# Kernel tuning notes

Hardware: AMD Instinct MI355X
Metric: run time of the kernel (lower is better)

Reference implementation:

```python
import jax, jax.numpy as jnp
import numpy as np

H = 20          # hidden_size
IN = 2          # GRU input / l1 output dim


def setup_inputs() -> dict:
    key = jax.random.key(0)
    ks = jax.random.split(key, 7)
    B = 32768
    s = 1.0 / np.sqrt(H)  # torch default init scale
    hidden = jax.random.normal(ks[0], (1, B, H), dtype=jnp.float32)
    w_ih = jax.random.uniform(ks[1], (3 * H, IN), jnp.float32, -s, s)
    w_hh = jax.random.uniform(ks[2], (3 * H, H), jnp.float32, -s, s)
    b_ih = jax.random.uniform(ks[3], (3 * H,), jnp.float32, -s, s)
    b_hh = jax.random.uniform(ks[4], (3 * H,), jnp.float32, -s, s)
    w_l = jax.random.uniform(ks[5], (IN, H), jnp.float32, -s, s)
    b_l = jax.random.uniform(ks[6], (IN,), jnp.float32, -s, s)
    return {"hidden": hidden, "w_ih": w_ih, "w_hh": w_hh,
            "b_ih": b_ih, "b_hh": b_hh, "w_l": w_l, "b_l": b_l,
            "step": 200}


def reference(hidden, w_ih, w_hh, b_ih, b_hh, w_l, b_l, step):
    reverse = True
    B = hidden.shape[1]
    h0 = hidden[0]                      # [B, H]
    x0 = jnp.zeros((B, IN), hidden.dtype)  # first GRU input is zeros

    def gru_step(carry, _):
        h, x = carry
        gi = x @ w_ih.T + b_ih          # [B, 3H]
        gh = h @ w_hh.T + b_hh          # [B, 3H]
        ir, iz, inn = jnp.split(gi, 3, axis=-1)
        hr, hz, hn = jnp.split(gh, 3, axis=-1)
        r = jax.nn.sigmoid(ir + hr)
        z = jax.nn.sigmoid(iz + hz)
        n = jnp.tanh(inn + r * hn)
        h_new = (1.0 - z) * n + z * h   # [B, H]
        y = h_new @ w_l.T + b_l         # [B, 2] -> next input
        return (h_new, y), y

    (_, _), ys = jax.lax.scan(gru_step, (h0, x0), None, length=step)
    # ys: [step, B, 2]; original appends per-step then reverses the list
    if reverse:
        ys = ys[::-1]
    return jnp.transpose(ys, (1, 0, 2))  # [B, step, 2]
```

## Files before the change

### kernel.cpp

```cpp
#include <hip/hip_runtime.h>

#define HDIM 20
#define BLOCK 256

typedef __fp16 half8 __attribute__((ext_vector_type(8)));
typedef __fp16 half2v __attribute__((ext_vector_type(2)));
typedef float  float4v __attribute__((ext_vector_type(4)));
typedef int    int4v  __attribute__((ext_vector_type(4)));

static __device__ __forceinline__ float4v mfma16(half8 a, half8 b, float4v c) {
    return __builtin_amdgcn_mfma_f32_16x16x32_f16(a, b, c, 0, 0, 0);
}


__global__ __launch_bounds__(BLOCK, 2) void gru_decoder_kernel(
    const float* __restrict__ hidden,
    const float* __restrict__ w_ih,
    const float* __restrict__ w_hh,
    const float* __restrict__ b_ih,
    const float* __restrict__ b_hh,
    const float* __restrict__ w_l,
    const float* __restrict__ b_l,
    const int*  __restrict__ step_ptr,
    float* __restrict__ out,
    int B)
{
    const int tid = threadIdx.x;
    const int l   = tid & 63;
    const int wv  = tid >> 6;
    const int el  = l & 15;
    const int q   = l >> 4;
    const int e   = (blockIdx.x * 4 + wv) * 16 + el;
    const int step = *step_ptr;

    const float NL2E  = -1.4426950408889634f;
    const float T2L2E =  2.8853900817779268f;

    const int u_dst = el >> 2;
    const int g     = el & 3;

    half8 Afold[5], Azero[5], Ay;
    #pragma unroll
    for (int T = 0; T < 5; ++T) {
        const int u  = 4 * T + u_dst;
        const int rr = (g == 0) ? u : (g == 1) ? 20 + u : 40 + u;
        const float sc = (g <= 1) ? NL2E : T2L2E;
        half8 hf, h0;
        #pragma unroll
        for (int j = 0; j < 8; ++j) {
            float af = 0.f, a0 = 0.f;
            if (j < 5) {
                const int uk = 4 * j + q;
                float wx = w_ih[rr * 2 + 0] * w_l[uk] + w_ih[rr * 2 + 1] * w_l[HDIM + uk];
                float wh = w_hh[rr * HDIM + uk];
                if (g <= 1)      { af = wh + wx; a0 = wh; }
                else if (g == 2) { af = wx;      a0 = 0.f; }
                else             { af = wh;      a0 = wh; }
            } else if (j == 7 && q == 0) {
                float bx = w_ih[rr * 2 + 0] * b_l[0] + w_ih[rr * 2 + 1] * b_l[1];
                if (g <= 1)      { af = b_ih[rr] + b_hh[rr] + bx; a0 = b_ih[rr] + b_hh[rr]; }
                else if (g == 2) { af = b_ih[rr] + bx;            a0 = b_ih[rr]; }
                else             { af = b_hh[rr];                 a0 = b_hh[rr]; }
            }
            hf[j] = (__fp16)(af * sc);
            h0[j] = (__fp16)(a0 * sc);
        }
        Afold[T] = hf;
        Azero[T] = h0;
    }
    {
        half8 hy;
        #pragma unroll
        for (int j = 0; j < 8; ++j) {
            float v = 0.f;
            if (el < 2) {
                if (j < 5)                 v = w_l[el * HDIM + 4 * j + q];
                else if (j == 7 && q == 0) v = b_l[el];
            }
            hy[j] = (__fp16)v;
        }
        Ay = hy;
    }

    int w3const;
    {
        half2v c67; c67[0] = (__fp16)0.f; c67[1] = (__fp16)((q == 0) ? 1.f : 0.f);
        w3const = __builtin_bit_cast(int, c67);
    }

    float hprev[5];
    half8 Bf;
    {
        const float* hb = hidden + (size_t)e * HDIM;
        #pragma unroll
        for (int T = 0; T < 5; ++T) hprev[T] = hb[4 * T + q];
        int4v bi;
        bi[0] = __builtin_bit_cast(int, __builtin_amdgcn_cvt_pkrtz(hprev[0], hprev[1]));
        bi[1] = __builtin_bit_cast(int, __builtin_amdgcn_cvt_pkrtz(hprev[2], hprev[3]));
        bi[2] = __builtin_bit_cast(int, __builtin_amdgcn_cvt_pkrtz(hprev[4], 0.f));
        bi[3] = w3const;
        Bf = __builtin_bit_cast(half8, bi);
    }

    const float4v czero = {0.f, 0.f, 0.f, 0.f};
    float4v C[5];

    auto issue_gates = [&](const half8* A) {
        #pragma unroll
        for (int T = 0; T < 5; ++T) C[T] = mfma16(A[T], Bf, czero);
    };
    auto finish_update = [&]() {
        #pragma unroll
        for (int T = 0; T < 5; ++T) {
            float r = __builtin_amdgcn_rcpf(1.f + __builtin_amdgcn_exp2f(C[T][0]));
            float z = __builtin_amdgcn_rcpf(1.f + __builtin_amdgcn_exp2f(C[T][1]));
            float npre2 = __builtin_fmaf(r, C[T][3], C[T][2]);
            float tn = __builtin_amdgcn_rcpf(1.f + __builtin_amdgcn_exp2f(npre2));
            float n = __builtin_fmaf(-2.f, tn, 1.f);
            hprev[T] = __builtin_fmaf(z, hprev[T] - n, n);
        }
        int4v bi;
        bi[0] = __builtin_bit_cast(int, __builtin_amdgcn_cvt_pkrtz(hprev[0], hprev[1]));
        bi[1] = __builtin_bit_cast(int, __builtin_amdgcn_cvt_pkrtz(hprev[2], hprev[3]));
        bi[2] = __builtin_bit_cast(int, __builtin_amdgcn_cvt_pkrtz(hprev[4], 0.f));
        bi[3] = w3const;
        Bf = __builtin_bit_cast(half8, bi);
    };

    float* outp = out + (size_t)e * 2 * step;

    issue_gates(Azero);
    finish_update();

    if ((step & 1) || step < 4) {
        for (int t = 1; t < step; ++t) {
            issue_gates(Afold);
            float4v cy = mfma16(Ay, Bf, czero);
            if (q == 0) {
                float2 st; st.x = cy[0]; st.y = cy[1];
                *(float2*)(outp + 2 * (step - t)) = st;
            }
            finish_update();
        }
        float4v cy = mfma16(Ay, Bf, czero);
        if (q == 0) {
            float2 st; st.x = cy[0]; st.y = cy[1];
            *(float2*)(outp) = st;
        }
        return;
    }

    float4v pend;
    float*  pendp;

    {
        issue_gates(Afold);
        float4v cyA = mfma16(Ay, Bf, czero);
        finish_update();
        issue_gates(Afold);
        float4v cyB = mfma16(Ay, Bf, czero);
        finish_update();
        pend[0] = cyB[0]; pend[1] = cyB[1]; pend[2] = cyA[0]; pend[3] = cyA[1];
        pendp = outp + 2 * (step - 2);
    }

    for (int k = step - 3; k >= 3; k -= 2) {
        issue_gates(Afold);
        float4v cyA = mfma16(Ay, Bf, czero);
        if (q == 0) *(float4v*)pendp = pend;
        finish_update();
        issue_gates(Afold);
        float4v cyB = mfma16(Ay, Bf, czero);
        finish_update();
        pend[0] = cyB[0]; pend[1] = cyB[1]; pend[2] = cyA[0]; pend[3] = cyA[1];
        pendp = outp + 2 * (k - 1);
    }

    {
        issue_gates(Afold);
        float4v cyA = mfma16(Ay, Bf, czero);
        if (q == 0) *(float4v*)pendp = pend;
        finish_update();
        float4v cyB = mfma16(Ay, Bf, czero);
        if (q == 0) {
            float4v st; st[0] = cyB[0]; st[1] = cyB[1]; st[2] = cyA[0]; st[3] = cyA[1];
            *(float4v*)outp = st;
        }
    }
}

extern "C" void kernel_launch(void* const* d_in, const int* in_sizes, int n_in,
                              void* d_out, int out_size, void* d_ws, size_t ws_size,
                              hipStream_t stream) {
    const float* hidden = (const float*)d_in[0];
    const float* w_ih   = (const float*)d_in[1];
    const float* w_hh   = (const float*)d_in[2];
    const float* b_ih   = (const float*)d_in[3];
    const float* b_hh   = (const float*)d_in[4];
    const float* w_l    = (const float*)d_in[5];
    const float* b_l    = (const float*)d_in[6];
    const int*   step   = (const int*)d_in[7];
    float* out = (float*)d_out;

    int B = in_sizes[0] / HDIM;
    int grid = B / 64;

    gru_decoder_kernel<<<grid, BLOCK, 0, stream>>>(
        hidden, w_ih, w_hh, b_ih, b_hh, w_l, b_l, step, out, B);
}
```

Measured before the change: 167.0 us.

## Batch reciprocals via shared-denominator trick and stagger block start with sleep

Rewrites the gate nonlinearity so that pairs of reciprocals share one rcp of their product, applied to the r/z sigmoids and to pairs of tanh denominators. This cuts transcendental-unit instructions per step in exchange for extra multiplies, and risks overflow when exp2 values are large, since the product of two denominators can reach inf. Odd groups of eight blocks also sleep briefly at start to desynchronise waves, so MFMA and transcendental phases interleave across waves on a CU.

```diff
diff --git a/kernel.cpp b/kernel.cpp
--- a/kernel.cpp
+++ b/kernel.cpp
@@ -110,14 +110,33 @@
         for (int T = 0; T < 5; ++T) C[T] = mfma16(A[T], Bf, czero);
     };
     auto finish_update = [&]() {
+        float zz[5], en[5];
         #pragma unroll
         for (int T = 0; T < 5; ++T) {
-            float r = __builtin_amdgcn_rcpf(1.f + __builtin_amdgcn_exp2f(C[T][0]));
-            float z = __builtin_amdgcn_rcpf(1.f + __builtin_amdgcn_exp2f(C[T][1]));
+            float er = __builtin_amdgcn_exp2f(C[T][0]);
+            float ez = __builtin_amdgcn_exp2f(C[T][1]);
+            float ar = 1.f + er;
+            float az = 1.f + ez;
+            float inv = __builtin_amdgcn_rcpf(ar * az);
+            float r  = az * inv;
+            zz[T]    = ar * inv;
             float npre2 = __builtin_fmaf(r, C[T][3], C[T][2]);
-            float tn = __builtin_amdgcn_rcpf(1.f + __builtin_amdgcn_exp2f(npre2));
-            float n = __builtin_fmaf(-2.f, tn, 1.f);
-            hprev[T] = __builtin_fmaf(z, hprev[T] - n, n);
+            en[T] = 1.f + __builtin_amdgcn_exp2f(npre2);
+        }
+        float tn[5];
+        {
+            float i01 = __builtin_amdgcn_rcpf(en[0] * en[1]);
+            tn[0] = en[1] * i01;
+            tn[1] = en[0] * i01;
+            float i23 = __builtin_amdgcn_rcpf(en[2] * en[3]);
+            tn[2] = en[3] * i23;
+            tn[3] = en[2] * i23;
+            tn[4] = __builtin_amdgcn_rcpf(en[4]);
+        }
+        #pragma unroll
+        for (int T = 0; T < 5; ++T) {
+            float n = __builtin_fmaf(-2.f, tn[T], 1.f);
+            hprev[T] = __builtin_fmaf(zz[T], hprev[T] - n, n);
         }
         int4v bi;
         bi[0] = __builtin_bit_cast(int, __builtin_amdgcn_cvt_pkrtz(hprev[0], hprev[1]));
@@ -128,6 +147,8 @@
     };
 
     float* outp = out + (size_t)e * 2 * step;
+
+    if ((blockIdx.x >> 3) & 1) __builtin_amdgcn_s_sleep(10);
 
     issue_gates(Azero);
     finish_update();
```

Result: no change. 169.0 us (+1.2%).

## Replace z and tanh transcendentals with shared-memory lookup tables

Applied to the files above, without the earlier changes.

Builds 64KB LDS lookup tables for sigmoid and tanh at kernel start. The weights are pre-scaled by 2048 and the MFMA accumulator gets an offset, so the z gate and the n-gate activation become a clamped byte offset plus one LDS load instead of exp2 and rcp. It also raises wave priority around the MFMA issue. The aim is fewer transcendental instructions on the serial recurrence path, at the cost of LDS latency and occupancy (64KB per block), quantization error from the 1/512 step and the fp16 scaled weights, and table-build overhead.

```diff
diff --git a/kernel.cpp b/kernel.cpp
--- a/kernel.cpp
+++ b/kernel.cpp
@@ -25,7 +25,19 @@
     float* __restrict__ out,
     int B)
 {
+    __shared__ float lut[16384];
+
     const int tid = threadIdx.x;
+
+    for (int i = tid; i < 8192; i += BLOCK) {
+        float x = (i - 4096) * (1.0f / 512.0f);
+        float es = __builtin_amdgcn_exp2f(-1.4426950408889634f * x);
+        lut[i] = __builtin_amdgcn_rcpf(1.f + es);
+        float et = __builtin_amdgcn_exp2f(2.8853900817779268f * x);
+        lut[8192 + i] = __builtin_fmaf(-2.f, __builtin_amdgcn_rcpf(1.f + et), 1.f);
+    }
+    __syncthreads();
+
     const int l   = tid & 63;
     const int wv  = tid >> 6;
     const int el  = l & 15;
@@ -34,7 +46,7 @@
     const int step = *step_ptr;
 
     const float NL2E  = -1.4426950408889634f;
-    const float T2L2E =  2.8853900817779268f;
+    const float BSCALE = 2048.0f;
 
     const int u_dst = el >> 2;
     const int g     = el & 3;
@@ -44,7 +56,7 @@
     for (int T = 0; T < 5; ++T) {
         const int u  = 4 * T + u_dst;
         const int rr = (g == 0) ? u : (g == 1) ? 20 + u : 40 + u;
-        const float sc = (g <= 1) ? NL2E : T2L2E;
+        const float sc = (g == 0) ? NL2E : BSCALE;
         half8 hf, h0;
         #pragma unroll
         for (int j = 0; j < 8; ++j) {
@@ -103,22 +115,40 @@
     }
 
     const float4v czero = {0.f, 0.f, 0.f, 0.f};
+    const float4v cinit = {0.f, 16386.f, 16386.f, 0.f};
+    const float  CLMAX = 32764.0f;
     float4v C[5];
 
     auto issue_gates = [&](const half8* A) {
-        #pragma unroll
-        for (int T = 0; T < 5; ++T) C[T] = mfma16(A[T], Bf, czero);
+        __builtin_amdgcn_s_setprio(1);
+        #pragma unroll
+        for (int T = 0; T < 5; ++T) C[T] = mfma16(A[T], Bf, cinit);
+        __builtin_amdgcn_s_setprio(0);
     };
+
+    const char* lbase = (const char*)lut;
+
     auto finish_update = [&]() {
+        float zz[5];
         #pragma unroll
         for (int T = 0; T < 5; ++T) {
-            float r = __builtin_amdgcn_rcpf(1.f + __builtin_amdgcn_exp2f(C[T][0]));
-            float z = __builtin_amdgcn_rcpf(1.f + __builtin_amdgcn_exp2f(C[T][1]));
-            float npre2 = __builtin_fmaf(r, C[T][3], C[T][2]);
-            float tn = __builtin_amdgcn_rcpf(1.f + __builtin_amdgcn_exp2f(npre2));
-            float n = __builtin_fmaf(-2.f, tn, 1.f);
-            hprev[T] = __builtin_fmaf(z, hprev[T] - n, n);
-        }
+            int bo = ((int)__builtin_amdgcn_fmed3f(C[T][1], 0.f, CLMAX)) & ~3;
+            zz[T] = *(const float*)(lbase + bo);
+        }
+        float rr_[5];
+        #pragma unroll
+        for (int T = 0; T < 5; ++T)
+            rr_[T] = __builtin_amdgcn_rcpf(1.f + __builtin_amdgcn_exp2f(C[T][0]));
+        float nn[5];
+        #pragma unroll
+        for (int T = 0; T < 5; ++T) {
+            float ui = __builtin_fmaf(rr_[T], C[T][3], C[T][2]);
+            int bo = ((int)__builtin_amdgcn_fmed3f(ui, 0.f, CLMAX)) & ~3;
+            nn[T] = *(const float*)(lbase + 32768 + bo);
+        }
+        #pragma unroll
+        for (int T = 0; T < 5; ++T)
+            hprev[T] = __builtin_fmaf(zz[T], hprev[T] - nn[T], nn[T]);
         int4v bi;
         bi[0] = __builtin_bit_cast(int, __builtin_amdgcn_cvt_pkrtz(hprev[0], hprev[1]));
         bi[1] = __builtin_bit_cast(int, __builtin_amdgcn_cvt_pkrtz(hprev[2], hprev[3]));
```

Result: faster. 158.8 us (-4.9%).
